# Performance work log

Hardware: AMD Instinct MI355X
Metric: run time of the kernel (lower is better)

## Reference

```python
import jax, jax.numpy as jnp
import numpy as np

N = 100000      # nodes
E = 1600000     # random edges (self loops added in reference, like add_self_loops)
D_IN = 128
D_OUT = 128
NEG_SLOPE = 0.01  # F.leaky_relu default in the torch source


def setup_inputs() -> dict:
    key = jax.random.key(0)
    k_x, k_e, k_w, k_b, k_a, k_ab = jax.random.split(key, 6)
    x = jax.random.normal(k_x, (N, D_IN), dtype=jnp.float32)
    edge_index = jax.random.randint(k_e, (2, E), 0, N, dtype=jnp.int32)
    # small init scales keep exp(score) in a sane range (torch default init is also small)
    W_lin = jax.random.normal(k_w, (D_OUT, D_IN), dtype=jnp.float32) * 0.05
    b_lin = jax.random.normal(k_b, (D_OUT,), dtype=jnp.float32) * 0.05
    W_att = jax.random.normal(k_a, (1, 2 * D_OUT), dtype=jnp.float32) * 0.05
    b_att = jax.random.normal(k_ab, (1,), dtype=jnp.float32) * 0.05
    return {"x": x, "edge_index": edge_index, "W_lin": W_lin, "b_lin": b_lin,
            "W_att": W_att, "b_att": b_att}


def reference(x, edge_index, W_lin, b_lin, W_att, b_att):
    n = x.shape[0]
    d_out = W_lin.shape[0]
    # h = lin(x), computed ONCE (the torch loop redundantly recomputes it per edge)
    h = x @ W_lin.T + b_lin                      # [N, D_OUT]
    # add self loops (pyg_utils.add_self_loops)
    loops = jnp.arange(n, dtype=edge_index.dtype)
    src = jnp.concatenate([edge_index[0], loops])  # node i (attends over its out-neighbors)
    dst = jnp.concatenate([edge_index[1], loops])  # neighbor j
    # attention([h_i ; h_j]) = h_i . a_i + h_j . a_j + b
    a_i = W_att[0, :d_out]
    a_j = W_att[0, d_out:]
    score = h[src] @ a_i + h[dst] @ a_j + b_att[0]           # [E+N]
    score = jnp.where(score >= 0, score, NEG_SLOPE * score)  # leaky_relu(0.01)
    e = jnp.exp(score)                                        # plain exp, as in source (no max-shift)
    denom = jax.ops.segment_sum(e, src, num_segments=n)       # per-source softmax denominator
    alpha = e / denom[src]                                    # [E+N]
    msg = alpha[:, None] * h[dst]                             # [E+N, D_OUT]
    agg = jax.ops.segment_sum(msg, src, num_segments=n)       # attention_matrix @ h
    return jax.nn.elu(agg)
```

## Files before the change

kernel.cpp:

```cpp
#include <hip/hip_runtime.h>
#include <hip/hip_bf16.h>
#include <stdint.h>

typedef unsigned int uint;
typedef unsigned short ushort;

#define D 128
#define NEG_SLOPE 0.01f
#define BN 64
#define CAP 1280
#define NCHUNK 768
#define KMAX 2048

using frag_t = __attribute__((ext_vector_type(8))) short;
using f32x4  = __attribute__((ext_vector_type(4))) float;

__device__ __forceinline__ ushort f2bf(float f) {
    __hip_bfloat16 b = __float2bfloat16(f);
    ushort u; __builtin_memcpy(&u, &b, 2); return u;
}
__device__ __forceinline__ float bflo(uint p) { return __uint_as_float(p << 16); }
__device__ __forceinline__ float bfhi(uint p) { return __uint_as_float(p & 0xffff0000u); }

#define LDK 136

__global__ __launch_bounds__(512) void gemm_h(
    const float* __restrict__ x, const float* __restrict__ W,
    const float* __restrict__ bias, const float* __restrict__ Wa,
    const float* __restrict__ ba,
    ushort* __restrict__ h, float* __restrict__ si, float* __restrict__ sj,
    const int* __restrict__ src, int* __restrict__ counts,
    int n, int e, int K, int cpb)
{
    __shared__ ushort xs[128 * LDK];
    __shared__ ushort wsh[128 * LDK];
    const int tid  = threadIdx.x;
    const int row0 = blockIdx.x * 128;

    {
        const int r = tid >> 5;
        const int k = (tid & 31) * 4;
#pragma unroll
        for (int i = 0; i < 8; ++i) {
            int lr = r + 16 * i;
            int gr = row0 + lr;
            int cr = gr < n ? gr : (n - 1);
            float4 v = *(const float4*)(x + (size_t)cr * D + k);
            ushort4 u; u.x = f2bf(v.x); u.y = f2bf(v.y); u.z = f2bf(v.z); u.w = f2bf(v.w);
            *(ushort4*)&xs[lr * LDK + k] = u;
        }
#pragma unroll
        for (int i = 0; i < 8; ++i) {
            int lr = r + 16 * i;
            float4 v = *(const float4*)(W + (size_t)lr * D + k);
            ushort4 u; u.x = f2bf(v.x); u.y = f2bf(v.y); u.z = f2bf(v.z); u.w = f2bf(v.w);
            *(ushort4*)&wsh[lr * LDK + k] = u;
        }
    }
    __syncthreads();

    const int wv   = tid >> 6;
    const int lane = tid & 63;
    const int mr   = lane & 15;
    const int qk   = (lane >> 4) * 8;

    f32x4 acc[8] = {};
    const ushort* xrow = xs + (16 * wv + mr) * LDK;
#pragma unroll
    for (int kk = 0; kk < 4; ++kk) {
        frag_t a = *(const frag_t*)(xrow + kk * 32 + qk);
#pragma unroll
        for (int t = 0; t < 8; ++t) {
            frag_t bf = *(const frag_t*)(wsh + (16 * t + mr) * LDK + kk * 32 + qk);
            acc[t] = __builtin_amdgcn_mfma_f32_16x16x32_bf16(a, bf, acc[t], 0, 0, 0);
        }
    }
    __syncthreads();

    const int crow = 16 * wv + (lane >> 4) * 4;
    float pi[4] = {0.f, 0.f, 0.f, 0.f};
    float pj[4] = {0.f, 0.f, 0.f, 0.f};
#pragma unroll
    for (int t = 0; t < 8; ++t) {
        int col = 16 * t + mr;
        float bb = bias[col];
        float av = Wa[col];
        float bv = Wa[D + col];
#pragma unroll
        for (int r = 0; r < 4; ++r) {
            float v = acc[t][r] + bb;
            int grow = row0 + crow + r;
            if (grow < n) h[(size_t)grow * D + col] = f2bf(v);
            pi[r] += v * av;
            pj[r] += v * bv;
        }
    }
#pragma unroll
    for (int o = 1; o < 16; o <<= 1) {
#pragma unroll
        for (int r = 0; r < 4; ++r) {
            pi[r] += __shfl_xor(pi[r], o);
            pj[r] += __shfl_xor(pj[r], o);
        }
    }
    if (mr == 0) {
        float bav = ba[0];
#pragma unroll
        for (int r = 0; r < 4; ++r) {
            int grow = row0 + crow + r;
            if (grow < n) { si[grow] = pi[r] + bav; sj[grow] = pj[r]; }
        }
    }

    const int c = blockIdx.x;
    if (c < NCHUNK) {
        int* hist = (int*)xs;
        for (int i = tid; i < K; i += 512) hist[i] = 0;
        __syncthreads();
        const int beg = c * cpb;
        const int end = min(e, beg + cpb);
        for (int i = beg + tid; i < end; i += 512)
            atomicAdd(&hist[src[i] >> 6], 1);
        __syncthreads();
        for (int i = tid; i < K; i += 512) counts[c * K + i] = hist[i];
    }
}

__global__ __launch_bounds__(NCHUNK) void scan_chunks(
    int* __restrict__ counts, int* __restrict__ total, int K)
{
    __shared__ int s[NCHUNK];
    const int b = blockIdx.x, t = threadIdx.x;
    int v = counts[t * K + b];
    s[t] = v; __syncthreads();
#pragma unroll
    for (int o = 1; o < NCHUNK; o <<= 1) {
        int tv = (t >= o) ? s[t - o] : 0;
        __syncthreads();
        s[t] += tv;
        __syncthreads();
    }
    counts[t * K + b] = s[t] - v;
    if (t == NCHUNK - 1) total[b] = s[t];
}

__global__ __launch_bounds__(512) void fill_k(
    const int* __restrict__ src, const int* __restrict__ dst,
    const int* __restrict__ cbase, uint* __restrict__ barr,
    int e, int K, int cpb)
{
    __shared__ int cur[KMAX];
    const int c = blockIdx.x;
    for (int i = threadIdx.x; i < K; i += 512) cur[i] = cbase[c * K + i];
    __syncthreads();
    const int beg = c * cpb;
    const int end = min(e, beg + cpb);
    for (int i = beg + threadIdx.x; i < end; i += 512) {
        int s = src[i], d = dst[i];
        int b = s >> 6;
        int p = atomicAdd(&cur[b], 1);
        if (p < CAP)
            barr[(size_t)b * CAP + p] = ((uint)(s & (BN - 1)) << 17) | (uint)d;
    }
}

__global__ __launch_bounds__(512) void agg_k(
    const ushort* __restrict__ h, const uint* __restrict__ barr,
    const int* __restrict__ total,
    const float* __restrict__ si, const float* __restrict__ sj,
    float* __restrict__ out, int n)
{
    __shared__ uint2 se[CAP];
    __shared__ int hist[BN];
    __shared__ int base[BN];
    __shared__ int cur[BN];
    __shared__ float si_s[BN];
    __shared__ float sj_s[BN];
    const int b    = blockIdx.x;
    const int tid  = threadIdx.x;
    const int lane = tid & 63;
    const int wv   = tid >> 6;
    const int node0 = b << 6;

    if (tid < BN) {
        hist[tid] = 0;
        int nd = node0 + tid;
        si_s[tid] = nd < n ? si[nd] : 0.f;
        sj_s[tid] = nd < n ? sj[nd] : 0.f;
    }
    __syncthreads();

    const int ecnt = min(total[b], CAP);
    const uint* eb = barr + (size_t)b * CAP;

    uint p0 = 0, p1 = 0, p2 = 0;
    float w0 = 0.f, w1 = 0.f, w2 = 0.f;
    const bool v0 = tid < ecnt, v1 = tid + 512 < ecnt, v2 = tid + 1024 < ecnt;
    if (v0) {
        p0 = eb[tid];
        float sc = si_s[p0 >> 17] + sj[p0 & 0x1FFFFu];
        sc = sc >= 0.f ? sc : NEG_SLOPE * sc;
        w0 = __expf(sc);
        atomicAdd(&hist[p0 >> 17], 1);
    }
    if (v1) {
        p1 = eb[tid + 512];
        float sc = si_s[p1 >> 17] + sj[p1 & 0x1FFFFu];
        sc = sc >= 0.f ? sc : NEG_SLOPE * sc;
        w1 = __expf(sc);
        atomicAdd(&hist[p1 >> 17], 1);
    }
    if (v2) {
        p2 = eb[tid + 1024];
        float sc = si_s[p2 >> 17] + sj[p2 & 0x1FFFFu];
        sc = sc >= 0.f ? sc : NEG_SLOPE * sc;
        w2 = __expf(sc);
        atomicAdd(&hist[p2 >> 17], 1);
    }
    __syncthreads();

    if (tid < 64) {
        int v = hist[tid];
        int s = v;
#pragma unroll
        for (int o = 1; o < 64; o <<= 1) {
            int t = __shfl_up(s, o);
            if (lane >= o) s += t;
        }
        base[tid] = s - v;
        cur[tid]  = s - v;
    }
    __syncthreads();

    if (v0) se[atomicAdd(&cur[p0 >> 17], 1)] = make_uint2(p0, __float_as_uint(w0));
    if (v1) se[atomicAdd(&cur[p1 >> 17], 1)] = make_uint2(p1, __float_as_uint(w1));
    if (v2) se[atomicAdd(&cur[p2 >> 17], 1)] = make_uint2(p2, __float_as_uint(w2));
    __syncthreads();

    const uint lo = (uint)lane << 1;
#pragma unroll 1
    for (int t = 0; t < 8; ++t) {
        const int ls = (wv << 3) + t;
        const int node = node0 + ls;
        if (node >= n) break;

        float sc = si_s[ls] + sj_s[ls];
        sc = sc >= 0.f ? sc : NEG_SLOPE * sc;
        float w_ = __expf(sc);
        uint hv = *(const uint*)(h + (((uint)node << 7) + lo));
        float a0 = w_ * bflo(hv), a1 = w_ * bfhi(hv);
        float denom = w_;

        const int c = hist[ls];
        const uint2* seg = se + base[ls];
        int j = 0;
        for (; j + 4 <= c; j += 4) {
            uint2 w0_ = seg[j], w1_ = seg[j + 1], w2_ = seg[j + 2], w3_ = seg[j + 3];
            uint g0 = *(const uint*)(h + (((w0_.x & 0x1FFFFu) << 7) + lo));
            uint g1 = *(const uint*)(h + (((w1_.x & 0x1FFFFu) << 7) + lo));
            uint g2 = *(const uint*)(h + (((w2_.x & 0x1FFFFu) << 7) + lo));
            uint g3 = *(const uint*)(h + (((w3_.x & 0x1FFFFu) << 7) + lo));
            float e0 = __uint_as_float(w0_.y), e1 = __uint_as_float(w1_.y);
            float e2 = __uint_as_float(w2_.y), e3 = __uint_as_float(w3_.y);
            denom += (e0 + e1) + (e2 + e3);
            a0 += e0 * bflo(g0) + e1 * bflo(g1) + e2 * bflo(g2) + e3 * bflo(g3);
            a1 += e0 * bfhi(g0) + e1 * bfhi(g1) + e2 * bfhi(g2) + e3 * bfhi(g3);
        }
        for (; j < c; ++j) {
            uint2 w = seg[j];
            uint g = *(const uint*)(h + (((w.x & 0x1FFFFu) << 7) + lo));
            float we = __uint_as_float(w.y);
            denom += we;
            a0 += we * bflo(g);
            a1 += we * bfhi(g);
        }

        float inv = 1.f / denom;
        a0 *= inv; a1 *= inv;
        a0 = a0 > 0.f ? a0 : expm1f(a0);
        a1 = a1 > 0.f ? a1 : expm1f(a1);
        *(float2*)(out + (((uint)node << 7) + lo)) = make_float2(a0, a1);
    }
}

extern "C" void kernel_launch(void* const* d_in, const int* in_sizes, int n_in,
                              void* d_out, int out_size, void* d_ws, size_t ws_size,
                              hipStream_t stream)
{
    const float* x  = (const float*)d_in[0];
    const int*   ei = (const int*)  d_in[1];
    const float* Wl = (const float*)d_in[2];
    const float* bl = (const float*)d_in[3];
    const float* Wa = (const float*)d_in[4];
    const float* ba = (const float*)d_in[5];
    const int n = in_sizes[0] / D;
    const int e = in_sizes[1] / 2;
    const int* src = ei;
    const int* dst = ei + e;

    const int K   = (n + BN - 1) / BN;
    const int cpb = (e + NCHUNK - 1) / NCHUNK;

    char* w = (char*)d_ws;
    size_t off = 0;
    ushort* h      = (ushort*)(w + off); off += (size_t)n * D * 2;
    float*  si     = (float*) (w + off); off += (size_t)n * 4;
    float*  sj     = (float*) (w + off); off += (size_t)n * 4;
    int*    counts = (int*)   (w + off); off += (size_t)NCHUNK * K * 4;
    int*    total  = (int*)   (w + off); off += ((size_t)K * 4 + 15) & ~(size_t)15;
    uint*   barr   = (uint*)  (w + off); off += (size_t)K * CAP * 4;

    const int gblocks = (n + 127) / 128;

    gemm_h      <<<gblocks, 512,    0, stream>>>(x, Wl, bl, Wa, ba, h, si, sj,
                                                 src, counts, n, e, K, cpb);
    scan_chunks <<<K,       NCHUNK, 0, stream>>>(counts, total, K);
    fill_k      <<<NCHUNK,  512,    0, stream>>>(src, dst, counts, barr, e, K, cpb);
    agg_k       <<<K,       512,    0, stream>>>(h, barr, total, si, sj, (float*)d_out, n);
}
```

Measured before the change: 244.9 us.

## Replace histogram-scan-fill pipeline with global atomic bucket reservation fused into GEMM launch

Removes the per-chunk count matrix, the scan kernel and the separate fill kernel. The first 256 blocks of a combined launch now build local histograms, reserve bucket slots with one global atomic per bucket (padded counters), and scatter the edges, while the remaining blocks run the GEMM. The GEMM also loads x straight into register fragments instead of staging it in shared memory, which shrinks LDS use. Edge order within each bucket now depends on atomic timing, so results are nondeterministic in floating-point summation order. A memset is added to zero the counters.

```diff
diff --git a/kernel.cpp b/kernel.cpp
--- a/kernel.cpp
+++ b/kernel.cpp
@@ -9,8 +9,9 @@
 #define NEG_SLOPE 0.01f
 #define BN 64
 #define CAP 1280
-#define NCHUNK 768
+#define NFILL 256
 #define KMAX 2048
+#define GSTRIDE 16
 
 using frag_t = __attribute__((ext_vector_type(8))) short;
 using f32x4  = __attribute__((ext_vector_type(4))) float;
@@ -24,58 +25,87 @@
 
 #define LDK 136
 
-__global__ __launch_bounds__(512) void gemm_h(
+__global__ __launch_bounds__(512) void gemm_fill(
     const float* __restrict__ x, const float* __restrict__ W,
     const float* __restrict__ bias, const float* __restrict__ Wa,
     const float* __restrict__ ba,
+    const int* __restrict__ src, const int* __restrict__ dst,
     ushort* __restrict__ h, float* __restrict__ si, float* __restrict__ sj,
-    const int* __restrict__ src, int* __restrict__ counts,
+    int* __restrict__ gcnt, uint* __restrict__ barr,
     int n, int e, int K, int cpb)
 {
-    __shared__ ushort xs[128 * LDK];
-    __shared__ ushort wsh[128 * LDK];
-    const int tid  = threadIdx.x;
-    const int row0 = blockIdx.x * 128;
-
-    {
-        const int r = tid >> 5;
-        const int k = (tid & 31) * 4;
-#pragma unroll
-        for (int i = 0; i < 8; ++i) {
-            int lr = r + 16 * i;
-            int gr = row0 + lr;
-            int cr = gr < n ? gr : (n - 1);
-            float4 v = *(const float4*)(x + (size_t)cr * D + k);
-            ushort4 u; u.x = f2bf(v.x); u.y = f2bf(v.y); u.z = f2bf(v.z); u.w = f2bf(v.w);
-            *(ushort4*)&xs[lr * LDK + k] = u;
-        }
-#pragma unroll
-        for (int i = 0; i < 8; ++i) {
-            int lr = r + 16 * i;
-            float4 v = *(const float4*)(W + (size_t)lr * D + k);
-            ushort4 u; u.x = f2bf(v.x); u.y = f2bf(v.y); u.z = f2bf(v.z); u.w = f2bf(v.w);
-            *(ushort4*)&wsh[lr * LDK + k] = u;
-        }
-    }
-    __syncthreads();
-
+    __shared__ union {
+        ushort wsh[128 * LDK];
+        int    cur[KMAX];
+    } sm;
+    const int tid = threadIdx.x;
+
+    if (blockIdx.x < NFILL) {
+        int* cur = sm.cur;
+        for (int i = tid; i < K; i += 512) cur[i] = 0;
+        __syncthreads();
+        const int beg = blockIdx.x * cpb;
+        const int end = min(e, beg + cpb);
+        for (int i = beg + tid; i < end; i += 512)
+            atomicAdd(&cur[src[i] >> 6], 1);
+        __syncthreads();
+        for (int i = tid; i < K; i += 512) {
+            int hc = cur[i];
+            cur[i] = hc ? atomicAdd(&gcnt[i * GSTRIDE], hc) : 0;
+        }
+        __syncthreads();
+        for (int i = beg + tid; i < end; i += 512) {
+            int s = src[i], d = dst[i];
+            int b = s >> 6;
+            int p = atomicAdd(&cur[b], 1);
+            if (p < CAP)
+                barr[(size_t)b * CAP + p] = ((uint)(s & (BN - 1)) << 17) | (uint)d;
+        }
+        return;
+    }
+
+    const int row0 = (blockIdx.x - NFILL) * 128;
     const int wv   = tid >> 6;
     const int lane = tid & 63;
     const int mr   = lane & 15;
     const int qk   = (lane >> 4) * 8;
 
+    {
+        const int r = tid >> 5;
+        const int k = (tid & 31) * 4;
+#pragma unroll
+        for (int i = 0; i < 8; ++i) {
+            int lr = r + 16 * i;
+            float4 v = *(const float4*)(W + lr * D + k);
+            ushort4 u; u.x = f2bf(v.x); u.y = f2bf(v.y); u.z = f2bf(v.z); u.w = f2bf(v.w);
+            *(ushort4*)&sm.wsh[lr * LDK + k] = u;
+        }
+    }
+
+    const int arow = row0 + 16 * wv + mr;
+    const int crd  = arow < n ? arow : (n - 1);
+    const float* xr = x + (size_t)crd * D + qk;
+    frag_t af[4];
+#pragma unroll
+    for (int kk = 0; kk < 4; ++kk) {
+        float4 u0 = *(const float4*)(xr + kk * 32);
+        float4 u1 = *(const float4*)(xr + kk * 32 + 4);
+        union { frag_t f; ushort us[8]; } c;
+        c.us[0] = f2bf(u0.x); c.us[1] = f2bf(u0.y); c.us[2] = f2bf(u0.z); c.us[3] = f2bf(u0.w);
+        c.us[4] = f2bf(u1.x); c.us[5] = f2bf(u1.y); c.us[6] = f2bf(u1.z); c.us[7] = f2bf(u1.w);
+        af[kk] = c.f;
+    }
+    __syncthreads();
+
     f32x4 acc[8] = {};
-    const ushort* xrow = xs + (16 * wv + mr) * LDK;
 #pragma unroll
     for (int kk = 0; kk < 4; ++kk) {
-        frag_t a = *(const frag_t*)(xrow + kk * 32 + qk);
 #pragma unroll
         for (int t = 0; t < 8; ++t) {
-            frag_t bf = *(const frag_t*)(wsh + (16 * t + mr) * LDK + kk * 32 + qk);
-            acc[t] = __builtin_amdgcn_mfma_f32_16x16x32_bf16(a, bf, acc[t], 0, 0, 0);
-        }
-    }
-    __syncthreads();
+            frag_t bf = *(const frag_t*)(sm.wsh + (16 * t + mr) * LDK + kk * 32 + qk);
+            acc[t] = __builtin_amdgcn_mfma_f32_16x16x32_bf16(af[kk], bf, acc[t], 0, 0, 0);
+        }
+    }
 
     const int crow = 16 * wv + (lane >> 4) * 4;
     float pi[4] = {0.f, 0.f, 0.f, 0.f};
@@ -111,62 +141,11 @@
             if (grow < n) { si[grow] = pi[r] + bav; sj[grow] = pj[r]; }
         }
     }
-
-    const int c = blockIdx.x;
-    if (c < NCHUNK) {
-        int* hist = (int*)xs;
-        for (int i = tid; i < K; i += 512) hist[i] = 0;
-        __syncthreads();
-        const int beg = c * cpb;
-        const int end = min(e, beg + cpb);
-        for (int i = beg + tid; i < end; i += 512)
-            atomicAdd(&hist[src[i] >> 6], 1);
-        __syncthreads();
-        for (int i = tid; i < K; i += 512) counts[c * K + i] = hist[i];
-    }
-}
-
-__global__ __launch_bounds__(NCHUNK) void scan_chunks(
-    int* __restrict__ counts, int* __restrict__ total, int K)
-{
-    __shared__ int s[NCHUNK];
-    const int b = blockIdx.x, t = threadIdx.x;
-    int v = counts[t * K + b];
-    s[t] = v; __syncthreads();
-#pragma unroll
-    for (int o = 1; o < NCHUNK; o <<= 1) {
-        int tv = (t >= o) ? s[t - o] : 0;
-        __syncthreads();
-        s[t] += tv;
-        __syncthreads();
-    }
-    counts[t * K + b] = s[t] - v;
-    if (t == NCHUNK - 1) total[b] = s[t];
-}
-
-__global__ __launch_bounds__(512) void fill_k(
-    const int* __restrict__ src, const int* __restrict__ dst,
-    const int* __restrict__ cbase, uint* __restrict__ barr,
-    int e, int K, int cpb)
-{
-    __shared__ int cur[KMAX];
-    const int c = blockIdx.x;
-    for (int i = threadIdx.x; i < K; i += 512) cur[i] = cbase[c * K + i];
-    __syncthreads();
-    const int beg = c * cpb;
-    const int end = min(e, beg + cpb);
-    for (int i = beg + threadIdx.x; i < end; i += 512) {
-        int s = src[i], d = dst[i];
-        int b = s >> 6;
-        int p = atomicAdd(&cur[b], 1);
-        if (p < CAP)
-            barr[(size_t)b * CAP + p] = ((uint)(s & (BN - 1)) << 17) | (uint)d;
-    }
 }
 
 __global__ __launch_bounds__(512) void agg_k(
     const ushort* __restrict__ h, const uint* __restrict__ barr,
-    const int* __restrict__ total,
+    const int* __restrict__ gcnt,
     const float* __restrict__ si, const float* __restrict__ sj,
     float* __restrict__ out, int n)
 {
@@ -190,7 +169,7 @@
     }
     __syncthreads();
 
-    const int ecnt = min(total[b], CAP);
+    const int ecnt = min(gcnt[b * GSTRIDE], CAP);
     const uint* eb = barr + (size_t)b * CAP;
 
     uint p0 = 0, p1 = 0, p2 = 0;
@@ -299,22 +278,20 @@
     const int* dst = ei + e;
 
     const int K   = (n + BN - 1) / BN;
-    const int cpb = (e + NCHUNK - 1) / NCHUNK;
+    const int cpb = (e + NFILL - 1) / NFILL;
 
     char* w = (char*)d_ws;
     size_t off = 0;
-    ushort* h      = (ushort*)(w + off); off += (size_t)n * D * 2;
-    float*  si     = (float*) (w + off); off += (size_t)n * 4;
-    float*  sj     = (float*) (w + off); off += (size_t)n * 4;
-    int*    counts = (int*)   (w + off); off += (size_t)NCHUNK * K * 4;
-    int*    total  = (int*)   (w + off); off += ((size_t)K * 4 + 15) & ~(size_t)15;
-    uint*   barr   = (uint*)  (w + off); off += (size_t)K * CAP * 4;
+    ushort* h    = (ushort*)(w + off); off += (size_t)n * D * 2;
+    float*  si   = (float*) (w + off); off += (size_t)n * 4;
+    float*  sj   = (float*) (w + off); off += (size_t)n * 4;
+    int*    gcnt = (int*)   (w + off); off += (size_t)K * GSTRIDE * 4;
+    uint*   barr = (uint*)  (w + off); off += (size_t)K * CAP * 4;
 
     const int gblocks = (n + 127) / 128;
 
-    gemm_h      <<<gblocks, 512,    0, stream>>>(x, Wl, bl, Wa, ba, h, si, sj,
-                                                 src, counts, n, e, K, cpb);
-    scan_chunks <<<K,       NCHUNK, 0, stream>>>(counts, total, K);
-    fill_k      <<<NCHUNK,  512,    0, stream>>>(src, dst, counts, barr, e, K, cpb);
-    agg_k       <<<K,       512,    0, stream>>>(h, barr, total, si, sj, (float*)d_out, n);
-}
+    hipMemsetAsync(gcnt, 0, (size_t)K * GSTRIDE * 4, stream);
+    gemm_fill <<<NFILL + gblocks, 512, 0, stream>>>(x, Wl, bl, Wa, ba, src, dst,
+                                                    h, si, sj, gcnt, barr, n, e, K, cpb);
+    agg_k     <<<K,               512, 0, stream>>>(h, barr, gcnt, si, sj, (float*)d_out, n);
+}
```

Result: faster. 235.1 us (-4.0%).
